# Kernel tuning notes

Measured on AMD Instinct MI355X. Metric: run time of the kernel, lower is better.

Reference implementation:

```python
import jax, jax.numpy as jnp
import numpy as np

# Crossbar analog-compute constants (match init_kwargs)
R_HRS = 1.0e6      # high-resistance state (ohms)
R_LRS = 1.0e4      # low-resistance state (ohms)
RP = 2.0           # parasitic wire resistance per segment (ohms)
BITS = 4           # conductance quantization bits
TS = 512           # max_array_size (tile size)
G_MIN = 1.0 / R_HRS
G_MAX = 1.0 / R_LRS


def weight_mapping(w):
    """Linearly map a weight tile to conductances in [G_MIN, G_MAX].
    Returns (cond, scale s, w_min) so the mapping can be inverted."""
    wmin = w.min()
    wmax = w.max()
    s = (G_MAX - G_MIN) / (wmax - wmin + 1e-12)
    cond = (w - wmin) * s + G_MIN
    return cond, s, wmin


def quantization(cond):
    """Quantize conductances to 2**BITS uniform levels in [G_MIN, G_MAX]."""
    n_levels = 2 ** BITS - 1
    step = (G_MAX - G_MIN) / n_levels
    return jnp.round((cond - G_MIN) / step) * step + G_MIN


def jeong_model(cond, x):
    """Nonlinear analog IV model: series parasitic wire resistance added per
    device position (Jeong-style approximation). cond: [ts_in, ts_out],
    x: [B, ts_in] -> currents [B, ts_out]."""
    ts_in, ts_out = cond.shape
    i = jnp.arange(ts_in, dtype=cond.dtype)[:, None]
    j = jnp.arange(ts_out, dtype=cond.dtype)[None, :]
    r_wire = RP * ((ts_in - i) + (j + 1.0))
    g_eff = 1.0 / (1.0 / cond + r_wire)
    return x @ g_eff


def ideal_model(cond, x):
    return x @ cond


def process_tile(w_tile, x_tile):
    """One crossbar tile: map -> quantize -> nonlinear IV -> correction -> unmap.
    w_tile: [TS, TS], x_tile: [B, TS] -> partial output [B, TS]."""
    cond, s, wmin = weight_mapping(w_tile)
    cond = quantization(cond)                      # bits>0 and non-ideal model
    currents = jeong_model(cond, x_tile)           # [B, TS]
    ideal = ideal_model(cond, x_tile)              # [B, TS]
    # correction: rescale nonlinear currents to the ideal dynamic range
    coeff = (ideal.max(axis=1) - ideal.min(axis=1)) / (
        currents.max(axis=1) - currents.min(axis=1) + 1e-8)
    currents = (currents - currents.mean(axis=1, keepdims=True)) * coeff[:, None] \
        + ideal.mean(axis=1, keepdims=True)
    # output_unmapping: invert cond = (w - wmin)*s + G_MIN given I = x @ cond
    offset = x_tile.sum(axis=1, keepdims=True) * (G_MIN - s * wmin)
    return (currents - offset) / s


def setup_inputs() -> dict:
    key = jax.random.key(0)
    kx, kw, kb = jax.random.split(key, 3)
    x = jax.random.normal(kx, (1024, 4096), dtype=jnp.float32)
    weight = jax.random.normal(kw, (4096, 4096), dtype=jnp.float32) * 0.05
    bias = jax.random.normal(kb, (4096,), dtype=jnp.float32) * 0.01
    return {"x": x, "weight": weight, "bias": bias}


def reference(x, weight, bias):
    B, in_features = x.shape
    _, out_features = weight.shape
    it, ot = in_features // TS, out_features // TS
    # weight tiles: [it, ot, TS, TS]; x tiles: [it, B, TS]
    w_tiles = weight.reshape(it, TS, ot, TS).transpose(0, 2, 1, 3)
    x_tiles = x.reshape(B, it, TS).transpose(1, 0, 2)
    tile_fn = jax.vmap(jax.vmap(process_tile, in_axes=(0, None)),  # over ot
                       in_axes=(0, 0))                             # over it
    parts = tile_fn(w_tiles, x_tiles)          # [it, ot, B, TS]
    out = parts.sum(axis=0)                    # [ot, B, TS]
    out = out.transpose(1, 0, 2).reshape(B, out_features)
    return out + bias
```

## Files before the change

### kernel.cpp

```cpp
#include <hip/hip_runtime.h>
#include <hip/hip_fp16.h>
#include <cstdint>

#define DI __device__ __forceinline__

typedef _Float16 f16;
typedef _Float16 half8 __attribute__((ext_vector_type(8)));
typedef float f32x4 __attribute__((ext_vector_type(4)));

constexpr int NF  = 4096;
constexpr int TSZ = 512;

constexpr float G_MIN  = (float)(1.0 / 1.0e6);
constexpr float GRANGE = (float)(1.0e-4 - 1.0e-6);
constexpr float QSTEP  = (float)((1.0e-4 - 1.0e-6) / 15.0);

__global__ __launch_bounds__(256)
void prep(const float* __restrict__ x, f16* __restrict__ xh,
          const float* __restrict__ w,
          float* __restrict__ pmin, float* __restrict__ pmax) {
    int bid = blockIdx.x;
    int t = threadIdx.x;
    if (bid < 4096) {
        int idx = bid * 256 + t;
        float4 v = ((const float4*)x)[idx];
        union { f16 h[4]; uint2 u; } o;
        o.h[0] = (f16)v.x; o.h[1] = (f16)v.y; o.h[2] = (f16)v.z; o.h[3] = (f16)v.w;
        ((uint2*)xh)[idx] = o.u;
        return;
    }
    int b2 = bid - 4096;
    int tile = b2 >> 4, sub = b2 & 15;
    int it = tile >> 3, jt = tile & 7;
    const float* base = w + (size_t)(it * TSZ + sub * 32) * NF + jt * TSZ;
    float mn = 3.4e38f, mx = -3.4e38f;
#pragma unroll
    for (int i = 0; i < 16; ++i) {
        int idx = i * 256 + t;
        int r = idx >> 7, c4 = idx & 127;
        float4 v = ((const float4*)(base + (size_t)r * NF))[c4];
        mn = fminf(mn, fminf(fminf(v.x, v.y), fminf(v.z, v.w)));
        mx = fmaxf(mx, fmaxf(fmaxf(v.x, v.y), fmaxf(v.z, v.w)));
    }
    for (int d = 1; d < 64; d <<= 1) {
        mn = fminf(mn, __shfl_xor(mn, d)); mx = fmaxf(mx, __shfl_xor(mx, d));
    }
    __shared__ float smn[4], smx[4];
    int wv = t >> 6;
    if ((t & 63) == 0) { smn[wv] = mn; smx[wv] = mx; }
    __syncthreads();
    if (t == 0) {
        pmin[b2] = fminf(fminf(smn[0], smn[1]), fminf(smn[2], smn[3]));
        pmax[b2] = fmaxf(fmaxf(smx[0], smx[1]), fmaxf(smx[2], smx[3]));
    }
}

__global__ void transform_w(const float* __restrict__ w,
                            const float* __restrict__ pmin, const float* __restrict__ pmax,
                            f16* __restrict__ wq_t, f16* __restrict__ h_t) {
#pragma clang fp contract(off)
    __shared__ f16 lwq[64][72];
    __shared__ f16 lh[64][72];
    int tile = blockIdx.x >> 6; int it = tile >> 3, jt = tile & 7;
    int sub = blockIdx.x & 63; int k0 = (sub >> 3) << 6, n0 = (sub & 7) << 6;
    float wmin = 3.4e38f, wmax = -3.4e38f;
#pragma unroll
    for (int u = 0; u < 16; ++u) {
        wmin = fminf(wmin, pmin[tile * 16 + u]);
        wmax = fmaxf(wmax, pmax[tile * 16 + u]);
    }
    float s = GRANGE / (wmax - wmin + 1e-12f);
    float inv_s = 1.0f / s;
    int t = threadIdx.x, cn = t & 63, r0 = t >> 6;
    for (int rr = 0; rr < 16; ++rr) {
        int rk = rr * 4 + r0;
        float wv = w[(size_t)(it * TSZ + k0 + rk) * NF + jt * TSZ + n0 + cn];
        float cond  = (wv - wmin) * s + G_MIN;
        float q     = rintf((cond - G_MIN) / QSTEP);
        float condq = q * QSTEP + G_MIN;
        float wqv   = (condq - G_MIN) * inv_s + wmin;
        float rw    = 2.0f * ((512.0f - (float)(k0 + rk)) + ((float)(n0 + cn) + 1.0f));
        float ge    = 1.0f / (1.0f / condq + rw);
        lwq[rk][cn] = (f16)wqv;
        lh[rk][cn]  = (f16)(ge * inv_s);
    }
    __syncthreads();
    for (int pp = 0; pp < 8; ++pp) {
        int nl = pp * 8 + (t >> 5);
        int kp = (t & 31) * 2;
        union { f16 h[2]; uint32_t u; } a, b;
        a.h[0] = lwq[kp][nl]; a.h[1] = lwq[kp + 1][nl];
        b.h[0] = lh[kp][nl];  b.h[1] = lh[kp + 1][nl];
        size_t obase = (size_t)tile * TSZ * TSZ + (size_t)(n0 + nl) * TSZ + k0 + kp;
        *(uint32_t*)(wq_t + obase) = a.u;
        *(uint32_t*)(h_t + obase)  = b.u;
    }
}

DI void gl16(const void* g, void* l) {
    auto gp = reinterpret_cast<const uint32_t __attribute__((address_space(1)))*>(
        reinterpret_cast<uintptr_t>(g));
    auto lp = reinterpret_cast<uint32_t __attribute__((address_space(3)))*>(
        reinterpret_cast<uintptr_t>(l));
    __builtin_amdgcn_global_load_lds(gp, lp, 16, 0, 0);
}

__global__ __launch_bounds__(256, 2)
void gemm_fused(const f16* __restrict__ A, const f16* __restrict__ B1,
                const f16* __restrict__ B2, f16* __restrict__ Qout,
                float* __restrict__ pmx, float* __restrict__ pmn, float* __restrict__ psm,
                float* __restrict__ qmx, float* __restrict__ qmn, float* __restrict__ qsm) {
    __shared__ __align__(16) f16 As[2][4096];
    __shared__ __align__(16) f16 B1s[2][4096];
    __shared__ __align__(16) f16 B2s[2][4096];
    __shared__ float sred[128][2][4];

    int bx = blockIdx.x;
    int tile = bx >> 5, mb = (bx >> 2) & 7, nb = bx & 3;
    int it = tile >> 3;
    int t = threadIdx.x, lane = t & 63, w = t >> 6;
    int wr = w >> 1, wc = w & 1;

    const f16* Ab  = A  + (size_t)(mb * 128) * NF + it * TSZ;
    const f16* B1b = B1 + ((size_t)tile * TSZ + nb * 128) * TSZ;
    const f16* B2b = B2 + ((size_t)tile * TSZ + nb * 128) * TSZ;

    int l1 = t, l2 = t + 256;
    int r1 = l1 >> 2, k1 = ((l1 & 3) ^ ((r1 >> 1) & 3)) * 8;
    int r2 = l2 >> 2, k2 = ((l2 & 3) ^ ((r2 >> 1) & 3)) * 8;
    const f16* a1  = Ab  + (size_t)r1 * NF  + k1;
    const f16* a2  = Ab  + (size_t)r2 * NF  + k2;
    const f16* b11 = B1b + (size_t)r1 * TSZ + k1;
    const f16* b12 = B1b + (size_t)r2 * TSZ + k2;
    const f16* b21 = B2b + (size_t)r1 * TSZ + k1;
    const f16* b22 = B2b + (size_t)r2 * TSZ + k2;

    f32x4 accP[4][4] = {};
    f32x4 accQ[4][4] = {};

    gl16(a1,  &As[0][w * 512]);  gl16(a2,  &As[0][2048 + w * 512]);
    gl16(b11, &B1s[0][w * 512]); gl16(b12, &B1s[0][2048 + w * 512]);
    gl16(b21, &B2s[0][w * 512]); gl16(b22, &B2s[0][2048 + w * 512]);
    a1 += 32; a2 += 32; b11 += 32; b12 += 32; b21 += 32; b22 += 32;
    __syncthreads();

    int rA = wr * 64 + (lane & 15);
    int rB = wc * 64 + (lane & 15);
    int sl = lane >> 4;

    for (int kt = 0; kt < 16; ++kt) {
        int cur = kt & 1, nxt = cur ^ 1;
        if (kt < 15) {
            gl16(a1,  &As[nxt][w * 512]);  gl16(a2,  &As[nxt][2048 + w * 512]);
            gl16(b11, &B1s[nxt][w * 512]); gl16(b12, &B1s[nxt][2048 + w * 512]);
            gl16(b21, &B2s[nxt][w * 512]); gl16(b22, &B2s[nxt][2048 + w * 512]);
            a1 += 32; a2 += 32; b11 += 32; b12 += 32; b21 += 32; b22 += 32;
        }
        half8 af[4], bf1[4], bf2[4];
#pragma unroll
        for (int m = 0; m < 4; ++m) {
            int row = rA + m * 16;
            af[m] = *(const half8*)&As[cur][row * 32 + ((sl ^ ((row >> 1) & 3)) << 3)];
        }
#pragma unroll
        for (int n = 0; n < 4; ++n) {
            int row = rB + n * 16;
            int o = row * 32 + ((sl ^ ((row >> 1) & 3)) << 3);
            bf1[n] = *(const half8*)&B1s[cur][o];
            bf2[n] = *(const half8*)&B2s[cur][o];
        }
#pragma unroll
        for (int m = 0; m < 4; ++m)
#pragma unroll
            for (int n = 0; n < 4; ++n) {
                accP[m][n] = __builtin_amdgcn_mfma_f32_16x16x32_f16(af[m], bf1[n], accP[m][n], 0, 0, 0);
                accQ[m][n] = __builtin_amdgcn_mfma_f32_16x16x32_f16(af[m], bf2[n], accQ[m][n], 0, 0, 0);
            }
        __syncthreads();
    }

#define ROW_STATS(ACC, DMX, DMN, DSM)                                          \
    {                                                                          \
        _Pragma("unroll")                                                      \
        for (int m = 0; m < 4; ++m) {                                          \
            _Pragma("unroll")                                                  \
            for (int r = 0; r < 4; ++r) {                                      \
                float mx = -3.4e38f, mn = 3.4e38f, sm = 0.f;                   \
                _Pragma("unroll")                                              \
                for (int n = 0; n < 4; ++n) {                                  \
                    float v = ACC[m][n][r];                                    \
                    mx = fmaxf(mx, v); mn = fminf(mn, v); sm += v;             \
                }                                                              \
                _Pragma("unroll")                                              \
                for (int d = 1; d < 16; d <<= 1) {                             \
                    mx = fmaxf(mx, __shfl_xor(mx, d));                         \
                    mn = fminf(mn, __shfl_xor(mn, d));                         \
                    sm += __shfl_xor(sm, d);                                   \
                }                                                              \
                if ((lane & 15) == 0) {                                        \
                    int row = wr * 64 + m * 16 + (lane >> 4) * 4 + r;          \
                    sred[row][wc][0] = mx; sred[row][wc][1] = mn;              \
                    sred[row][wc][2] = sm;                                     \
                }                                                              \
            }                                                                  \
        }                                                                      \
        __syncthreads();                                                       \
        if (t < 128) {                                                         \
            float mx = fmaxf(sred[t][0][0], sred[t][1][0]);                    \
            float mn = fminf(sred[t][0][1], sred[t][1][1]);                    \
            float sm = sred[t][0][2] + sred[t][1][2];                          \
            size_t idx = ((size_t)tile * 1024 + mb * 128 + t) * 4 + nb;        \
            DMX[idx] = mx; DMN[idx] = mn; DSM[idx] = sm;                       \
        }                                                                      \
        __syncthreads();                                                       \
    }

    ROW_STATS(accP, pmx, pmn, psm)
    ROW_STATS(accQ, qmx, qmn, qsm)
#undef ROW_STATS

    size_t base = ((size_t)tile * 1024 + mb * 128) * 512 + nb * 128;
#pragma unroll
    for (int m = 0; m < 4; ++m) {
        int row0 = wr * 64 + m * 16 + (lane >> 4) * 4;
#pragma unroll
        for (int n = 0; n < 4; ++n) {
            int col = wc * 64 + n * 16 + (lane & 15);
#pragma unroll
            for (int r = 0; r < 4; ++r)
                Qout[base + (size_t)(row0 + r) * 512 + col] = (f16)accQ[m][n][r];
        }
    }
}

__global__ __launch_bounds__(256)
void combine(const f16* __restrict__ Q,
             const float* __restrict__ pmx, const float* __restrict__ pmn,
             const float* __restrict__ psm,
             const float* __restrict__ qmx, const float* __restrict__ qmn,
             const float* __restrict__ qsm,
             const float* __restrict__ pmin1, const float* __restrict__ pmax1,
             const float* __restrict__ bias, float* __restrict__ out) {
    int bid = blockIdx.x;
    int jt = bid & 7, b = bid >> 3;
    int t = threadIdx.x;

    uint32_t qv[8];
#pragma unroll
    for (int i = 0; i < 8; ++i) {
        int tile = i * 8 + jt;
        qv[i] = ((const uint32_t*)(Q + ((size_t)tile * 1024 + b) * 512))[t];
    }
    float2 bv = ((const float2*)(bias + jt * 512))[t];

    float alpha_r[8], beta_r[8];
#pragma unroll
    for (int i = 0; i < 8; ++i) {
        int tile = i * 8 + jt;
        float wmn = 3.4e38f, wmx = -3.4e38f;
#pragma unroll
        for (int u = 0; u < 16; ++u) {
            wmn = fminf(wmn, pmin1[tile * 16 + u]);
            wmx = fmaxf(wmx, pmax1[tile * 16 + u]);
        }
        float s = GRANGE / (wmx - wmn + 1e-12f);
        size_t p = ((size_t)tile * 1024 + b) * 4;
        float pmax = fmaxf(fmaxf(pmx[p], pmx[p+1]), fmaxf(pmx[p+2], pmx[p+3]));
        float pmin = fminf(fminf(pmn[p], pmn[p+1]), fminf(pmn[p+2], pmn[p+3]));
        float psum = psm[p] + psm[p+1] + psm[p+2] + psm[p+3];
        float qmax = fmaxf(fmaxf(qmx[p], qmx[p+1]), fmaxf(qmx[p+2], qmx[p+3]));
        float qmin = fminf(fminf(qmn[p], qmn[p+1]), fminf(qmn[p+2], qmn[p+3]));
        float qsum = qsm[p] + qsm[p+1] + qsm[p+2] + qsm[p+3];
        float coeff = (s * (pmax - pmin)) / (s * (qmax - qmin) + 1e-8f);
        float meanP = psum * (1.0f / 512.0f);
        float meanQ = qsum * (1.0f / 512.0f);
        alpha_r[i] = coeff;
        beta_r[i]  = meanP - coeff * meanQ;
    }

    float o0 = 0.f, o1 = 0.f, bsum = 0.f;
#pragma unroll
    for (int i = 0; i < 8; ++i) {
        union { uint32_t u; f16 h[2]; } q2; q2.u = qv[i];
        o0 = fmaf(alpha_r[i], (float)q2.h[0], o0);
        o1 = fmaf(alpha_r[i], (float)q2.h[1], o1);
        bsum += beta_r[i];
    }
    float2 ov; ov.x = o0 + bsum + bv.x; ov.y = o1 + bsum + bv.y;
    ((float2*)(out + (size_t)b * 4096))[jt * 256 + t] = ov;
}

extern "C" void kernel_launch(void* const* d_in, const int* in_sizes, int n_in,
                              void* d_out, int out_size, void* d_ws, size_t ws_size,
                              hipStream_t stream) {
    const float* x    = (const float*)d_in[0];
    const float* wt   = (const float*)d_in[1];
    const float* bias = (const float*)d_in[2];
    float* out = (float*)d_out;
    char* ws = (char*)d_ws;

    float* pmin1 = (float*)ws;
    float* pmax1 = (float*)(ws + 4096);
    size_t off = 8192;
    f16* xh   = (f16*)(ws + off); off += (size_t)1024 * 4096 * 2;
    f16* wq_t = (f16*)(ws + off); off += (size_t)4096 * 4096 * 2;
    f16* h_t  = (f16*)(ws + off); off += (size_t)4096 * 4096 * 2;
    float* pmx = (float*)(ws + off); off += (size_t)64 * 1024 * 4 * 4;
    float* pmn = (float*)(ws + off); off += (size_t)64 * 1024 * 4 * 4;
    float* psm = (float*)(ws + off); off += (size_t)64 * 1024 * 4 * 4;
    float* qmx = (float*)(ws + off); off += (size_t)64 * 1024 * 4 * 4;
    float* qmn = (float*)(ws + off); off += (size_t)64 * 1024 * 4 * 4;
    float* qsm = (float*)(ws + off); off += (size_t)64 * 1024 * 4 * 4;
    f16* Q    = (f16*)(ws + off);

    prep        <<<5120, 256, 0, stream>>>(x, xh, wt, pmin1, pmax1);
    transform_w <<<4096, 256, 0, stream>>>(wt, pmin1, pmax1, wq_t, h_t);
    gemm_fused  <<<2048, 256, 0, stream>>>(xh, wq_t, h_t, Q,
                                           pmx, pmn, psm, qmx, qmn, qsm);
    combine     <<<8192, 256, 0, stream>>>(Q, pmx, pmn, psm, qmx, qmn, qsm,
                                           pmin1, pmax1, bias, out);
}
```

Before: 336.1 us.

## Enlarge GEMM block tile to 256 rows and precompute per-row alpha/beta

The fused dual GEMM now runs 512-thread blocks covering 256 batch rows instead of 128, so each B1/B2 weight tile loaded into LDS is reused across twice as many rows and the number of blocks is halved. Shared memory becomes a single 64 KB buffer that is reused for the row-stat reduction. The per-row correction coefficients move out of combine into a small alphabeta kernel, so they are computed once per (tile,row) instead of by every thread of each combine block. The cost is higher LDS use per block, which may limit occupancy, plus one extra kernel launch.

```diff
diff --git a/kernel.cpp b/kernel.cpp
--- a/kernel.cpp
+++ b/kernel.cpp
@@ -105,43 +105,43 @@
     __builtin_amdgcn_global_load_lds(gp, lp, 16, 0, 0);
 }
 
-__global__ __launch_bounds__(256, 2)
+__global__ __launch_bounds__(512, 4)
 void gemm_fused(const f16* __restrict__ A, const f16* __restrict__ B1,
                 const f16* __restrict__ B2, f16* __restrict__ Qout,
                 float* __restrict__ pmx, float* __restrict__ pmn, float* __restrict__ psm,
                 float* __restrict__ qmx, float* __restrict__ qmn, float* __restrict__ qsm) {
-    __shared__ __align__(16) f16 As[2][4096];
-    __shared__ __align__(16) f16 B1s[2][4096];
-    __shared__ __align__(16) f16 B2s[2][4096];
-    __shared__ float sred[128][2][4];
+    __shared__ __align__(16) char smem[65536];
+    f16* As  = (f16*)smem;
+    f16* B1s = (f16*)(smem + 32768);
+    f16* B2s = (f16*)(smem + 49152);
+    float* sred = (float*)smem;
 
     int bx = blockIdx.x;
-    int tile = bx >> 5, mb = (bx >> 2) & 7, nb = bx & 3;
+    int tile = bx >> 4, mb = (bx >> 2) & 3, nb = bx & 3;
     int it = tile >> 3;
     int t = threadIdx.x, lane = t & 63, w = t >> 6;
     int wr = w >> 1, wc = w & 1;
 
-    const f16* Ab  = A  + (size_t)(mb * 128) * NF + it * TSZ;
+    const f16* Ab  = A  + (size_t)(mb * 256) * NF + it * TSZ;
     const f16* B1b = B1 + ((size_t)tile * TSZ + nb * 128) * TSZ;
     const f16* B2b = B2 + ((size_t)tile * TSZ + nb * 128) * TSZ;
 
-    int l1 = t, l2 = t + 256;
-    int r1 = l1 >> 2, k1 = ((l1 & 3) ^ ((r1 >> 1) & 3)) * 8;
-    int r2 = l2 >> 2, k2 = ((l2 & 3) ^ ((r2 >> 1) & 3)) * 8;
-    const f16* a1  = Ab  + (size_t)r1 * NF  + k1;
-    const f16* a2  = Ab  + (size_t)r2 * NF  + k2;
-    const f16* b11 = B1b + (size_t)r1 * TSZ + k1;
-    const f16* b12 = B1b + (size_t)r2 * TSZ + k2;
-    const f16* b21 = B2b + (size_t)r1 * TSZ + k1;
-    const f16* b22 = B2b + (size_t)r2 * TSZ + k2;
+    int la1 = t, la2 = t + 512;
+    int ra1 = la1 >> 2, ka1 = ((la1 & 3) ^ ((ra1 >> 1) & 3)) * 8;
+    int ra2 = la2 >> 2, ka2 = ((la2 & 3) ^ ((ra2 >> 1) & 3)) * 8;
+    int rb  = t >> 2,   kb  = ((t & 3) ^ ((rb >> 1) & 3)) * 8;
+    const f16* a1 = Ab  + (size_t)ra1 * NF  + ka1;
+    const f16* a2 = Ab  + (size_t)ra2 * NF  + ka2;
+    const f16* b1 = B1b + (size_t)rb  * TSZ + kb;
+    const f16* b2 = B2b + (size_t)rb  * TSZ + kb;
 
     f32x4 accP[4][4] = {};
     f32x4 accQ[4][4] = {};
 
-    gl16(a1,  &As[0][w * 512]);  gl16(a2,  &As[0][2048 + w * 512]);
-    gl16(b11, &B1s[0][w * 512]); gl16(b12, &B1s[0][2048 + w * 512]);
-    gl16(b21, &B2s[0][w * 512]); gl16(b22, &B2s[0][2048 + w * 512]);
-    a1 += 32; a2 += 32; b11 += 32; b12 += 32; b21 += 32; b22 += 32;
+    int wb = w * 512;
+    gl16(a1, As + wb);  gl16(a2, As + 4096 + wb);
+    gl16(b1, B1s + wb); gl16(b2, B2s + wb);
+    a1 += 32; a2 += 32; b1 += 32; b2 += 32;
     __syncthreads();
 
     int rA = wr * 64 + (lane & 15);
@@ -151,23 +151,22 @@
     for (int kt = 0; kt < 16; ++kt) {
         int cur = kt & 1, nxt = cur ^ 1;
         if (kt < 15) {
-            gl16(a1,  &As[nxt][w * 512]);  gl16(a2,  &As[nxt][2048 + w * 512]);
-            gl16(b11, &B1s[nxt][w * 512]); gl16(b12, &B1s[nxt][2048 + w * 512]);
-            gl16(b21, &B2s[nxt][w * 512]); gl16(b22, &B2s[nxt][2048 + w * 512]);
-            a1 += 32; a2 += 32; b11 += 32; b12 += 32; b21 += 32; b22 += 32;
+            gl16(a1, As + nxt * 8192 + wb);  gl16(a2, As + nxt * 8192 + 4096 + wb);
+            gl16(b1, B1s + nxt * 4096 + wb); gl16(b2, B2s + nxt * 4096 + wb);
+            a1 += 32; a2 += 32; b1 += 32; b2 += 32;
         }
         half8 af[4], bf1[4], bf2[4];
 #pragma unroll
         for (int m = 0; m < 4; ++m) {
             int row = rA + m * 16;
-            af[m] = *(const half8*)&As[cur][row * 32 + ((sl ^ ((row >> 1) & 3)) << 3)];
+            af[m] = *(const half8*)&As[cur * 8192 + row * 32 + ((sl ^ ((row >> 1) & 3)) << 3)];
         }
 #pragma unroll
         for (int n = 0; n < 4; ++n) {
             int row = rB + n * 16;
             int o = row * 32 + ((sl ^ ((row >> 1) & 3)) << 3);
-            bf1[n] = *(const half8*)&B1s[cur][o];
-            bf2[n] = *(const half8*)&B2s[cur][o];
+            bf1[n] = *(const half8*)&B1s[cur * 4096 + o];
+            bf2[n] = *(const half8*)&B2s[cur * 4096 + o];
         }
 #pragma unroll
         for (int m = 0; m < 4; ++m)
@@ -199,17 +198,18 @@
                 }                                                              \
                 if ((lane & 15) == 0) {                                        \
                     int row = wr * 64 + m * 16 + (lane >> 4) * 4 + r;          \
-                    sred[row][wc][0] = mx; sred[row][wc][1] = mn;              \
-                    sred[row][wc][2] = sm;                                     \
+                    sred[(row * 2 + wc) * 3 + 0] = mx;                         \
+                    sred[(row * 2 + wc) * 3 + 1] = mn;                         \
+                    sred[(row * 2 + wc) * 3 + 2] = sm;                         \
                 }                                                              \
             }                                                                  \
         }                                                                      \
         __syncthreads();                                                       \
-        if (t < 128) {                                                         \
-            float mx = fmaxf(sred[t][0][0], sred[t][1][0]);                    \
-            float mn = fminf(sred[t][0][1], sred[t][1][1]);                    \
-            float sm = sred[t][0][2] + sred[t][1][2];                          \
-            size_t idx = ((size_t)tile * 1024 + mb * 128 + t) * 4 + nb;        \
+        if (t < 256) {                                                         \
+            float mx = fmaxf(sred[(t * 2) * 3 + 0], sred[(t * 2 + 1) * 3 + 0]);\
+            float mn = fminf(sred[(t * 2) * 3 + 1], sred[(t * 2 + 1) * 3 + 1]);\
+            float sm = sred[(t * 2) * 3 + 2] + sred[(t * 2 + 1) * 3 + 2];      \
+            size_t idx = ((size_t)tile * 1024 + mb * 256 + t) * 4 + nb;        \
             DMX[idx] = mx; DMN[idx] = mn; DSM[idx] = sm;                       \
         }                                                                      \
         __syncthreads();                                                       \
@@ -219,7 +219,7 @@
     ROW_STATS(accQ, qmx, qmn, qsm)
 #undef ROW_STATS
 
-    size_t base = ((size_t)tile * 1024 + mb * 128) * 512 + nb * 128;
+    size_t base = ((size_t)tile * 1024 + mb * 256) * 512 + nb * 128;
 #pragma unroll
     for (int m = 0; m < 4; ++m) {
         int row0 = wr * 64 + m * 16 + (lane >> 4) * 4;
@@ -233,59 +233,55 @@
     }
 }
 
+__global__ void alphabeta(const float* __restrict__ pmx, const float* __restrict__ pmn,
+                          const float* __restrict__ psm,
+                          const float* __restrict__ qmx, const float* __restrict__ qmn,
+                          const float* __restrict__ qsm,
+                          const float* __restrict__ pmin1, const float* __restrict__ pmax1,
+                          float* __restrict__ alpha, float* __restrict__ beta) {
+    int i = blockIdx.x * 256 + threadIdx.x;
+    int tile = i >> 10;
+    float wmn = 3.4e38f, wmx = -3.4e38f;
+#pragma unroll
+    for (int u = 0; u < 16; ++u) {
+        wmn = fminf(wmn, pmin1[tile * 16 + u]);
+        wmx = fmaxf(wmx, pmax1[tile * 16 + u]);
+    }
+    float s = GRANGE / (wmx - wmn + 1e-12f);
+    size_t p = (size_t)i * 4;
+    float pmax = fmaxf(fmaxf(pmx[p], pmx[p+1]), fmaxf(pmx[p+2], pmx[p+3]));
+    float pmin = fminf(fminf(pmn[p], pmn[p+1]), fminf(pmn[p+2], pmn[p+3]));
+    float psum = psm[p] + psm[p+1] + psm[p+2] + psm[p+3];
+    float qmax = fmaxf(fmaxf(qmx[p], qmx[p+1]), fmaxf(qmx[p+2], qmx[p+3]));
+    float qmin = fminf(fminf(qmn[p], qmn[p+1]), fminf(qmn[p+2], qmn[p+3]));
+    float qsum = qsm[p] + qsm[p+1] + qsm[p+2] + qsm[p+3];
+    float coeff = (s * (pmax - pmin)) / (s * (qmax - qmin) + 1e-8f);
+    float meanP = psum * (1.0f / 512.0f);
+    float meanQ = qsum * (1.0f / 512.0f);
+    alpha[i] = coeff;
+    beta[i]  = meanP - coeff * meanQ;
+}
+
 __global__ __launch_bounds__(256)
 void combine(const f16* __restrict__ Q,
-             const float* __restrict__ pmx, const float* __restrict__ pmn,
-             const float* __restrict__ psm,
-             const float* __restrict__ qmx, const float* __restrict__ qmn,
-             const float* __restrict__ qsm,
-             const float* __restrict__ pmin1, const float* __restrict__ pmax1,
+             const float* __restrict__ alpha, const float* __restrict__ beta,
              const float* __restrict__ bias, float* __restrict__ out) {
     int bid = blockIdx.x;
     int jt = bid & 7, b = bid >> 3;
     int t = threadIdx.x;
-
-    uint32_t qv[8];
+    float o0 = 0.f, o1 = 0.f, bsum = 0.f;
 #pragma unroll
     for (int i = 0; i < 8; ++i) {
         int tile = i * 8 + jt;
-        qv[i] = ((const uint32_t*)(Q + ((size_t)tile * 1024 + b) * 512))[t];
+        int ab = tile * 1024 + b;
+        float a = alpha[ab];
+        bsum += beta[ab];
+        union { uint32_t u; f16 h[2]; } q2;
+        q2.u = ((const uint32_t*)(Q + ((size_t)tile * 1024 + b) * 512))[t];
+        o0 = fmaf(a, (float)q2.h[0], o0);
+        o1 = fmaf(a, (float)q2.h[1], o1);
     }
     float2 bv = ((const float2*)(bias + jt * 512))[t];
-
-    float alpha_r[8], beta_r[8];
-#pragma unroll
-    for (int i = 0; i < 8; ++i) {
-        int tile = i * 8 + jt;
-        float wmn = 3.4e38f, wmx = -3.4e38f;
-#pragma unroll
-        for (int u = 0; u < 16; ++u) {
-            wmn = fminf(wmn, pmin1[tile * 16 + u]);
-            wmx = fmaxf(wmx, pmax1[tile * 16 + u]);
-        }
-        float s = GRANGE / (wmx - wmn + 1e-12f);
-        size_t p = ((size_t)tile * 1024 + b) * 4;
-        float pmax = fmaxf(fmaxf(pmx[p], pmx[p+1]), fmaxf(pmx[p+2], pmx[p+3]));
-        float pmin = fminf(fminf(pmn[p], pmn[p+1]), fminf(pmn[p+2], pmn[p+3]));
-        float psum = psm[p] + psm[p+1] + psm[p+2] + psm[p+3];
-        float qmax = fmaxf(fmaxf(qmx[p], qmx[p+1]), fmaxf(qmx[p+2], qmx[p+3]));
-        float qmin = fminf(fminf(qmn[p], qmn[p+1]), fminf(qmn[p+2], qmn[p+3]));
-        float qsum = qsm[p] + qsm[p+1] + qsm[p+2] + qsm[p+3];
-        float coeff = (s * (pmax - pmin)) / (s * (qmax - qmin) + 1e-8f);
-        float meanP = psum * (1.0f / 512.0f);
-        float meanQ = qsum * (1.0f / 512.0f);
-        alpha_r[i] = coeff;
-        beta_r[i]  = meanP - coeff * meanQ;
-    }
-
-    float o0 = 0.f, o1 = 0.f, bsum = 0.f;
-#pragma unroll
-    for (int i = 0; i < 8; ++i) {
-        union { uint32_t u; f16 h[2]; } q2; q2.u = qv[i];
-        o0 = fmaf(alpha_r[i], (float)q2.h[0], o0);
-        o1 = fmaf(alpha_r[i], (float)q2.h[1], o1);
-        bsum += beta_r[i];
-    }
     float2 ov; ov.x = o0 + bsum + bv.x; ov.y = o1 + bsum + bv.y;
     ((float2*)(out + (size_t)b * 4096))[jt * 256 + t] = ov;
 }
@@ -311,12 +307,15 @@
     float* qmx = (float*)(ws + off); off += (size_t)64 * 1024 * 4 * 4;
     float* qmn = (float*)(ws + off); off += (size_t)64 * 1024 * 4 * 4;
     float* qsm = (float*)(ws + off); off += (size_t)64 * 1024 * 4 * 4;
+    float* alpha = (float*)(ws + off); off += (size_t)64 * 1024 * 4;
+    float* beta  = (float*)(ws + off); off += (size_t)64 * 1024 * 4;
     f16* Q    = (f16*)(ws + off);
 
     prep        <<<5120, 256, 0, stream>>>(x, xh, wt, pmin1, pmax1);
     transform_w <<<4096, 256, 0, stream>>>(wt, pmin1, pmax1, wq_t, h_t);
-    gemm_fused  <<<2048, 256, 0, stream>>>(xh, wq_t, h_t, Q,
+    gemm_fused  <<<1024, 512, 0, stream>>>(xh, wq_t, h_t, Q,
                                            pmx, pmn, psm, qmx, qmn, qsm);
-    combine     <<<8192, 256, 0, stream>>>(Q, pmx, pmn, psm, qmx, qmn, qsm,
-                                           pmin1, pmax1, bias, out);
-}
+    alphabeta   <<<256,  256, 0, stream>>>(pmx, pmn, psm, qmx, qmn, qsm,
+                                           pmin1, pmax1, alpha, beta);
+    combine     <<<8192, 256, 0, stream>>>(Q, alpha, beta, bias, out);
+}
```

Result: slower. 753.3 us (+124.1%).
